# Kernel tuning notes

Hardware: AMD Instinct MI355X
Metric: run time of the kernel (lower is better)

The kernel has to match this reference:

```python
import jax, jax.numpy as jnp
import numpy as np

B, DIN, NU, N, ORDER = 256, 64, 256, 207, 3
KC = (ORDER + 1) * (DIN + NU)  # 1280 concat channels into gate conv
SQRT_D = float(np.sqrt(NU))


def layer_norm(x, w, b, eps=1e-5):
    mu = jnp.mean(x, -1, keepdims=True)
    var = jnp.mean((x - mu) ** 2, -1, keepdims=True)
    return (x - mu) / jnp.sqrt(var + eps) * w + b


def spatial_diffusion(x, adj, order):
    # x: (B, C, N). Order-K diffusion with self term, matching SpatialConvOrderK:
    # x_k[..., w] = sum_v adj[w, v] * x_{k-1}[..., v]
    outs = [x]
    xk = x
    for _ in range(order):
        xk = jnp.einsum('bcv,wv->bcw', xk, adj)
        outs.append(xk)
    return jnp.concatenate(outs, axis=1)  # (B, (order+1)*C, N)


def transformer_layer(s, in_proj_w, in_proj_b, out_proj_w, out_proj_b,
                      ln1_w, ln1_b, ln2_w, ln2_b, ffn_w1, ffn_b1, ffn_w2, ffn_b2):
    # s: (N, B, d). Single-head post-LN TransformerEncoderLayer, eval mode (dropout off).
    qkv = s @ in_proj_w.T + in_proj_b
    q, k, v = jnp.split(qkv, 3, axis=-1)
    attn = jax.nn.softmax(jnp.einsum('nbd,mbd->bnm', q, k) / SQRT_D, axis=-1)
    o = jnp.einsum('bnm,mbd->nbd', attn, v) @ out_proj_w.T + out_proj_b
    s = layer_norm(s + o, ln1_w, ln1_b)
    f = jax.nn.relu(s @ ffn_w1.T + ffn_b1) @ ffn_w2.T + ffn_b2
    return layer_norm(s + f, ln2_w, ln2_b)


def gcgru_forward(x, delta_t, h, adj, mask_last_tp, embed,
                  in_proj_w, in_proj_b, out_proj_w, out_proj_b,
                  ln1_w, ln1_b, ln2_w, ln2_b, ffn_w1, ffn_b1, ffn_w2, ffn_b2,
                  W_u, b_u, W_c, b_c, step):
    if step != 0:
        h_p = jnp.transpose(h, (2, 0, 1))  # (N, B, NU)
        inp = h_p + embed[:, None, :] * jnp.transpose(mask_last_tp, (2, 0, 1))  # (N,B,1) bcast
        eps = jnp.tanh(transformer_layer(inp, in_proj_w, in_proj_b, out_proj_w, out_proj_b,
                                         ln1_w, ln1_b, ln2_w, ln2_b,
                                         ffn_w1, ffn_b1, ffn_w2, ffn_b2))
        eps = jnp.transpose(eps, (1, 2, 0))  # (B, NU, N)
        dt = delta_t[..., None]  # (B, 1, 1)
        h = jnp.sqrt(1.0 - dt) * h - jnp.sqrt(dt) * eps
    xg = jnp.concatenate([x, h], axis=1)  # (B, DIN+NU, N)
    # update_gate and c_gate receive the identical concat -> compute diffusion once
    z = spatial_diffusion(xg, adj, ORDER)  # (B, KC, N)
    u = jax.nn.sigmoid(jnp.einsum('bcn,oc->bon', z, W_u) + b_u[None, :, None])
    c = jnp.tanh(jnp.einsum('bcn,oc->bon', z, W_c) + b_c[None, :, None])
    return u * h + (1.0 - u) * c


def setup_inputs() -> dict:
    key = jax.random.key(0)
    ks = jax.random.split(key, 16)
    d = NU

    def nrm(k, shape, s=0.02):
        return jax.random.normal(k, shape, jnp.float32) * s

    return dict(
        x=jax.random.normal(ks[0], (B, DIN, N), jnp.float32),
        delta_t=jax.random.uniform(ks[1], (B, 1), jnp.float32, 0.01, 0.99),
        h=jax.random.normal(ks[2], (B, NU, N), jnp.float32),
        adj=jax.random.uniform(ks[3], (N, N), jnp.float32) / N,
        mask=jnp.ones((B, 1, N), jnp.float32),
        mask_last_tp=(jax.random.uniform(ks[4], (B, 1, N)) > 0.5).astype(jnp.float32),
        time_encoding=jnp.zeros((B, d), jnp.float32),
        step=1,
        embed=nrm(ks[5], (N, d), 1.0),
        in_proj_w=nrm(ks[6], (3 * d, d)), in_proj_b=jnp.zeros((3 * d,), jnp.float32),
        out_proj_w=nrm(ks[7], (d, d)), out_proj_b=jnp.zeros((d,), jnp.float32),
        ln1_w=jnp.ones((d,), jnp.float32), ln1_b=jnp.zeros((d,), jnp.float32),
        ln2_w=jnp.ones((d,), jnp.float32), ln2_b=jnp.zeros((d,), jnp.float32),
        ffn_w1=nrm(ks[8], (d, d)), ffn_b1=jnp.zeros((d,), jnp.float32),
        ffn_w2=nrm(ks[9], (d, d)), ffn_b2=jnp.zeros((d,), jnp.float32),
        W_u=nrm(ks[10], (NU, KC)), b_u=jnp.zeros((NU,), jnp.float32),
        W_c=nrm(ks[11], (NU, KC)), b_c=jnp.zeros((NU,), jnp.float32),
    )


def reference(x, delta_t, h, adj, mask, mask_last_tp, time_encoding, step,
              embed, in_proj_w, in_proj_b, out_proj_w, out_proj_b,
              ln1_w, ln1_b, ln2_w, ln2_b, ffn_w1, ffn_b1, ffn_w2, ffn_b2,
              W_u, b_u, W_c, b_c):
    # mask / time_encoding are accepted but unused, exactly as in the torch epsilon.forward
    return gcgru_forward(x, delta_t, h, adj, mask_last_tp, embed,
                         in_proj_w, in_proj_b, out_proj_w, out_proj_b,
                         ln1_w, ln1_b, ln2_w, ln2_b, ffn_w1, ffn_b1, ffn_w2, ffn_b2,
                         W_u, b_u, W_c, b_c, step)
```

## Files before the change

### kernel.cpp

```cpp
#include <hip/hip_runtime.h>
#include <hip/hip_bf16.h>

typedef __hip_bfloat16 bf16;
typedef __attribute__((ext_vector_type(8))) short s8v;
typedef __attribute__((ext_vector_type(4))) short s4v;
typedef __attribute__((ext_vector_type(4))) float f4v;

#define MFMA(a, b, c) __builtin_amdgcn_mfma_f32_16x16x32_bf16(a, b, c, 0, 0, 0)

#define B_    256
#define DIN_  64
#define NU_   256
#define NN_   207
#define KC_   1280
#define NB_   (NN_ * B_)
#define NBD_  13565952LL

#define WU_OFF   0LL
#define WC_OFF   327680LL
#define IP_OFF   655360LL
#define OP_OFF   851968LL
#define F1_OFF   917504LL
#define F2_OFF   983040LL
#define ADJ_OFF  1048576LL
#define WEXT_N   (ADJ_OFF + 207LL * 256LL)

__device__ __forceinline__ float bf2f(bf16 v) { return __bfloat162float(v); }
__device__ __forceinline__ bf16  f2bf(float v) { return __float2bfloat16(v); }
__device__ __forceinline__ short f2s(float v) { bf16 t = __float2bfloat16(v); return *(short*)&t; }

__device__ __forceinline__ void gl16(const void* g, void* l) {
    __builtin_amdgcn_global_load_lds(
        (const __attribute__((address_space(1))) void*)g,
        (__attribute__((address_space(3))) void*)l, 16, 0, 0);
}

#define SWZ(rr, cb) ((rr) * 64 + ((((cb) + q) ^ ((rr) & 7)) << 3))

__global__ __launch_bounds__(256) void cvt_w_k(
    const float* __restrict__ Wu, const float* __restrict__ Wc,
    const float* __restrict__ ip, const float* __restrict__ op,
    const float* __restrict__ f1, const float* __restrict__ f2,
    const float* __restrict__ adj, short* __restrict__ dst)
{
    long long t = (long long)blockIdx.x * 256 + threadIdx.x;
    long long nt = (long long)gridDim.x * 256;
    for (long long g = t; g < 262144; g += nt) {
        long long e = g * 4;
        const float* src; long long off;
        if (e < WC_OFF)      { src = Wu; off = e; }
        else if (e < IP_OFF) { src = Wc; off = e - WC_OFF; }
        else if (e < OP_OFF) { src = ip; off = e - IP_OFF; }
        else if (e < F1_OFF) { src = op; off = e - OP_OFF; }
        else if (e < F2_OFF) { src = f1; off = e - F1_OFF; }
        else                 { src = f2; off = e - F2_OFF; }
        float4 fv = *(const float4*)(src + off);
        s4v v = {f2s(fv.x), f2s(fv.y), f2s(fv.z), f2s(fv.w)};
        *(s4v*)(dst + e) = v;
    }
    short* adst = dst + ADJ_OFF;
    for (long long g = t; g < 207LL * 256LL; g += nt) {
        int r = (int)(g >> 8), c = (int)(g & 255);
        adst[g] = (c < NN_) ? f2s(adj[r * NN_ + c]) : (short)0;
    }
}

template<int EPI>
__global__ __launch_bounds__(256, 3) void gemm128(
    const short* __restrict__ A, int lda,
    const short* __restrict__ Wb, int ldb,
    const float* __restrict__ bias, bf16* __restrict__ C, int ldc,
    int K, int act, short* __restrict__ vt,
    const float* __restrict__ bu, const float* __restrict__ bc,
    const bf16* __restrict__ hnT, float* __restrict__ outF)
{
    __shared__ __align__(16) short Tiles[2][128 * 64];
    short* As = Tiles[0];
    short* Bs = Tiles[1];
    float* outS = (float*)&Tiles[0][0];
    const int w_ = blockIdx.y * gridDim.x + blockIdx.x;
    const int nswz = gridDim.x;
    const int xr = w_ & 7, sidx = w_ >> 3;
    const int mt = xr + 8 * (sidx / nswz);
    const int nt = sidx % nswz;
    if (mt >= 414) return;
    const int m0 = mt * 128, n0 = nt * 128;
    const int tid = threadIdx.x;
    const int lane = tid & 63, wid = tid >> 6;
    const int l15 = lane & 15, q = lane >> 4;
    const int wm = (wid >> 1) * 64, wn = (wid & 1) * 64;
    const int seg_r = lane >> 3;
    const int csw8 = ((lane & 7) ^ seg_r) << 3;
    const int nk = K >> 6;

    const short* ap[4];
    const short* bp[4];
#pragma unroll
    for (int i = 0; i < 4; i++) {
        int gm = m0 + (wid * 4 + i) * 8 + seg_r;
        ap[i] = A + (long long)gm * lda + csw8;
        int gn = n0 + (wid * 4 + i) * 8 + seg_r;
        int pr = EPI ? ((gn & 1) * 256 + (gn >> 1)) : gn;
        bp[i] = Wb + (long long)pr * ldb + csw8;
    }

    f4v acc[4][4] = {};

    for (int t = 0; t < nk; ++t) {
        const int k0 = t << 6;
#pragma unroll
        for (int i = 0; i < 4; i++) {
            gl16(ap[i] + k0, &As[(wid * 4 + i) * 512]);
            gl16(bp[i] + k0, &Bs[(wid * 4 + i) * 512]);
        }
        __syncthreads();
#pragma unroll
        for (int ks = 0; ks < 64; ks += 32) {
            const int cb = ks >> 3;
            s8v af[4], bfv[4];
#pragma unroll
            for (int i = 0; i < 4; i++) {
                int rr = wm + i * 16 + l15;
                af[i] = *(const s8v*)&As[SWZ(rr, cb)];
            }
#pragma unroll
            for (int j = 0; j < 4; j++) {
                int rr = wn + j * 16 + l15;
                bfv[j] = *(const s8v*)&Bs[SWZ(rr, cb)];
            }
#pragma unroll
            for (int i = 0; i < 4; i++)
#pragma unroll
                for (int j = 0; j < 4; j++)
                    acc[i][j] = MFMA(af[i], bfv[j], acc[i][j]);
        }
        __syncthreads();
    }

    if (EPI == 0) {
#pragma unroll
        for (int i = 0; i < 4; i++) {
            int mbase = m0 + wm + i * 16 + q * 4;
#pragma unroll
            for (int j = 0; j < 4; j++) {
                int n = n0 + wn + j * 16 + l15;
                float bv = bias ? bias[n] : 0.f;
#pragma unroll
                for (int r = 0; r < 4; r++) {
                    int m = mbase + r;
                    float v = acc[i][j][r] + bv;
                    if (act == 3) v = fmaxf(v, 0.f);
                    if (vt && n >= 512) {
                        int d = n - 512;
                        int bb = m / NN_;
                        int node = m - bb * NN_;
                        vt[((long long)bb * 256 + d) * 208 + node] = f2s(v);
                    } else {
                        C[(long long)m * ldc + n] = f2bf(v);
                    }
                }
            }
        }
    } else {
        const int odd = l15 & 1;
#pragma unroll
        for (int i = 0; i < 4; i++) {
            int mlbase = wm + i * 16 + q * 4;
#pragma unroll
            for (int j = 0; j < 4; j++) {
                int n = n0 + wn + j * 16 + l15;
                int och = n >> 1;
                int ochl = (wn + j * 16 + l15) >> 1;
                float bv = odd ? bc[och] : bu[och];
#pragma unroll
                for (int r = 0; r < 4; r++) {
                    int ml = mlbase + r;
                    float pre = acc[i][j][r] + bv;
                    float myv;
                    if (odd) {
                        float e = __expf(2.f * pre);
                        myv = (e - 1.f) / (e + 1.f);
                    } else {
                        myv = 1.f / (1.f + __expf(-pre));
                    }
                    float oth = __shfl_xor(myv, 1);
                    if (!odd) {
                        int m = m0 + ml;
                        float hv = bf2f(hnT[(long long)m * 256 + och]);
                        float res = myv * hv + (1.f - myv) * oth;
                        outS[ochl * 128 + (ml ^ ((ochl & 7) << 2))] = res;
                    }
                }
            }
        }
        __syncthreads();
        for (int orow = tid >> 6; orow < 64; orow += 4) {
            int och = (n0 >> 1) + orow;
            const int sx = (orow & 7) << 2;
#pragma unroll
            for (int half = 0; half < 2; half++) {
                int ml = lane + half * 64;
                float v = outS[orow * 128 + (ml ^ sx)];
                int m = m0 + ml;
                int bb = m / NN_;
                int node = m - bb * NN_;
                outF[((long long)bb * NU_ + och) * NN_ + node] = v;
            }
        }
    }
}

__global__ __launch_bounds__(256) void gemm_nk0(
    const short* __restrict__ A, int lda,
    const float* __restrict__ Wf, int ldb,
    const float* __restrict__ bias, bf16* __restrict__ C, int ldc,
    int M, int N, int K, int act, short* __restrict__ vt)
{
    __shared__ __align__(16) short As[2][128 * 64];
    __shared__ __align__(16) short Bs[2][128 * 64];
    const int tid = threadIdx.x;
    const int lane = tid & 63, wid = tid >> 6;
    const int l15 = lane & 15, q = lane >> 4;
    const int wm = (wid >> 1) * 64, wn = (wid & 1) * 64;
    const int m0 = blockIdx.y * 128, n0 = blockIdx.x * 128;

    f4v acc[4][4] = {};
    const int nk = K >> 6;

    auto stage = [&](int k0, int pb) {
#pragma unroll
        for (int i = 0; i < 4; i++) {
            int idx = tid + (i << 8);
            int r = idx >> 3, c = idx & 7;
            int gm = m0 + r, gk = k0 + (c << 3);
            s8v v = {0, 0, 0, 0, 0, 0, 0, 0};
            if (gm < M) v = *(const s8v*)(A + (long long)gm * lda + gk);
            *(s8v*)&As[pb][r * 64 + ((c ^ (r & 7)) << 3)] = v;
        }
#pragma unroll
        for (int i = 0; i < 8; i++) {
            int idx = tid + (i << 8);
            int r = idx >> 4, c4 = idx & 15;
            int gn = n0 + r, gk = k0 + (c4 << 2);
            s4v v = {0, 0, 0, 0};
            if (gn < N) {
                float4 fx = *(const float4*)(Wf + (long long)gn * ldb + gk);
                v[0] = f2s(fx.x); v[1] = f2s(fx.y); v[2] = f2s(fx.z); v[3] = f2s(fx.w);
            }
            *(s4v*)&Bs[pb][r * 64 + (((c4 >> 1) ^ (r & 7)) << 3) + ((c4 & 1) << 2)] = v;
        }
    };

    stage(0, 0);
    __syncthreads();
    int pp = 0;
    for (int t = 0; t < nk; ++t) {
        if (t + 1 < nk) stage((t + 1) << 6, pp ^ 1);
#pragma unroll
        for (int ks = 0; ks < 64; ks += 32) {
            const int cb = ks >> 3;
            s8v af[4], bfv[4];
#pragma unroll
            for (int i = 0; i < 4; i++) {
                int rr = wm + i * 16 + l15;
                af[i] = *(const s8v*)&As[pp][SWZ(rr, cb)];
            }
#pragma unroll
            for (int j = 0; j < 4; j++) {
                int rr = wn + j * 16 + l15;
                bfv[j] = *(const s8v*)&Bs[pp][SWZ(rr, cb)];
            }
#pragma unroll
            for (int i = 0; i < 4; i++)
#pragma unroll
                for (int j = 0; j < 4; j++)
                    acc[i][j] = MFMA(af[i], bfv[j], acc[i][j]);
        }
        __syncthreads();
        pp ^= 1;
    }

#pragma unroll
    for (int i = 0; i < 4; i++) {
        int mbase = m0 + wm + i * 16 + q * 4;
#pragma unroll
        for (int j = 0; j < 4; j++) {
            int n = n0 + wn + j * 16 + l15;
            if (n >= N) continue;
            float bv = bias ? bias[n] : 0.f;
#pragma unroll
            for (int r = 0; r < 4; r++) {
                int m = mbase + r;
                if (m >= M) continue;
                float v = acc[i][j][r] + bv;
                if (act == 3) v = fmaxf(v, 0.f);
                if (vt && n >= 512) {
                    int d = n - 512;
                    int bb = m / NN_;
                    int node = m - bb * NN_;
                    vt[((long long)bb * 256 + d) * 208 + node] = f2s(v);
                } else {
                    C[(long long)m * ldc + n] = f2bf(v);
                }
            }
        }
    }
}

__global__ __launch_bounds__(256) void attn_k(
    const short* __restrict__ qk, const short* __restrict__ vt,
    bf16* __restrict__ ao)
{
    __shared__ __align__(16) short Plds[64 * 232];
    __shared__ float sums[64];
    const int tid = threadIdx.x;
    const int lane = tid & 63, w = tid >> 6;
    const int l15 = lane & 15, quad = lane >> 4;
    const int w_ = blockIdx.y * gridDim.x + blockIdx.x;
    const int xr = w_ & 7, sidx = w_ >> 3;
    const int b = xr + 8 * (sidx >> 2);
    const int q0 = (sidx & 3) * 64;
    const long long rowcap = (long long)NB_ - 1;

    long long qrow = (long long)b * NN_ + q0 + w * 16 + l15;
    if (qrow > rowcap) qrow = rowcap;
    const short* qp = qk + qrow * 512;
    s8v bq[8];
#pragma unroll
    for (int ks = 0; ks < 8; ks++)
        bq[ks] = *(const s8v*)(qp + ks * 32 + quad * 8);

    const short* jp[13];
#pragma unroll
    for (int jf = 0; jf < 13; jf++) {
        long long jrow = (long long)b * NN_ + jf * 16 + l15;
        if (jrow > rowcap) jrow = rowcap;
        jp[jf] = qk + jrow * 512 + 256;
    }

    f4v sacc[13] = {};
#pragma unroll
    for (int ks = 0; ks < 8; ks++) {
        const int off = ks * 32 + quad * 8;
#pragma unroll
        for (int jf = 0; jf < 13; jf++) {
            s8v a = *(const s8v*)(jp[jf] + off);
            sacc[jf] = MFMA(a, bq[ks], sacc[jf]);
        }
    }

    float mx = -3.0e38f;
    float pv[13][4];
#pragma unroll
    for (int jf = 0; jf < 13; jf++)
#pragma unroll
        for (int r = 0; r < 4; r++) {
            int j = jf * 16 + quad * 4 + r;
            float v = (j < NN_) ? sacc[jf][r] * 0.0625f : -3.0e38f;
            pv[jf][r] = v;
            mx = fmaxf(mx, v);
        }
    mx = fmaxf(mx, __shfl_xor(mx, 16));
    mx = fmaxf(mx, __shfl_xor(mx, 32));
    float sum = 0.f;
#pragma unroll
    for (int jf = 0; jf < 13; jf++)
#pragma unroll
        for (int r = 0; r < 4; r++) {
            float p = __expf(pv[jf][r] - mx);
            pv[jf][r] = p;
            sum += p;
        }
    sum += __shfl_xor(sum, 16);
    sum += __shfl_xor(sum, 32);

    const int qloc = w * 16 + l15;
#pragma unroll
    for (int jf = 0; jf < 13; jf++)
#pragma unroll
        for (int r = 0; r < 4; r++)
            Plds[qloc * 232 + jf * 16 + quad * 4 + r] = f2s(pv[jf][r]);
    if (quad == 0) sums[qloc] = 1.f / sum;
#pragma unroll
    for (int i = 0; i < 4; i++) {
        int u = tid + i * 256;
        Plds[(u >> 4) * 232 + 208 + (u & 15)] = 0;
    }
    __syncthreads();

    const short* vbase = vt + (long long)b * 256 * 208;
    f4v oacc[16] = {};
#pragma unroll
    for (int ks = 0; ks < 7; ks++) {
        s8v pa = *(const s8v*)&Plds[(w * 16 + l15) * 232 + ks * 32 + quad * 8];
#pragma unroll
        for (int df = 0; df < 16; df++) {
            s8v vb = *(const s8v*)(vbase + (df * 16 + l15) * 208 + ks * 32 + quad * 8);
            oacc[df] = MFMA(pa, vb, oacc[df]);
        }
    }

#pragma unroll
    for (int df = 0; df < 16; df++) {
        int d = df * 16 + l15;
#pragma unroll
        for (int r = 0; r < 4; r++) {
            int ql = w * 16 + quad * 4 + r;
            int qg = q0 + ql;
            if (qg < NN_)
                ao[((long long)b * NN_ + qg) * 256 + d] = f2bf(oacc[df][r] * sums[ql]);
        }
    }
}

template<int WB>
__global__ __launch_bounds__(256) void diff_k(
    const float* __restrict__ adj, const short* __restrict__ adjb,
    const short* __restrict__ zT_in,
    short* __restrict__ zT_out, int col_in, int col_out)
{
    __shared__ __align__(16) short As[2][128 * 64];
    __shared__ __align__(16) short Bs[2][128 * 64];
    const int tid = threadIdx.x;
    const int lane = tid & 63, wid = tid >> 6;
    const int l15 = lane & 15, q = lane >> 4;
    const int wm = (wid >> 1) * 64, wn = (wid & 1) * 64;
    const int m0 = blockIdx.y * 128, n0 = blockIdx.x * 128;
    const long long zb = (long long)blockIdx.z * NN_ * KC_;
    const int seg_r = lane >> 3, chunk = lane & 7;
    const int csw8 = (chunk ^ seg_r) << 3;
    const int bv_ = tid & 63, bcg = tid >> 6;

    f4v acc[4][4] = {};

    auto stageA = [&](int k0, int pb) {
        if (WB) {
#pragma unroll
            for (int i = 0; i < 4; i++) {
                int seg = wid * 4 + i;
                int gm = m0 + seg * 8 + seg_r;
                if (gm > NN_ - 1) gm = NN_ - 1;
                gl16(adjb + gm * 256 + k0 + csw8, &As[pb][seg * 512]);
            }
        } else {
#pragma unroll
            for (int i = 0; i < 32; i++) {
                int idx = tid + (i << 8);
                int r = idx >> 6, c = idx & 63;
                int gm = m0 + r, gk = k0 + c;
                short vv = (gm < NN_ && gk < NN_) ? f2s(adj[gm * NN_ + gk]) : (short)0;
                As[pb][r * 64 + (((c >> 3) ^ (r & 7)) << 3) + (c & 7)] = vv;
            }
        }
    };
    auto loadB = [&](int k0, s8v* breg) {
#pragma unroll
        for (int i = 0; i < 4; i++) {
            int gv = k0 + bv_, gc = n0 + (bcg + i * 4) * 8;
            s8v val = {0, 0, 0, 0, 0, 0, 0, 0};
            if (gv < NN_ && gc < 320)
                val = *(const s8v*)&zT_in[zb + (long long)gv * KC_ + col_in + gc];
            breg[i] = val;
        }
    };
    auto writeB = [&](s8v* breg, int pb) {
#pragma unroll
        for (int i = 0; i < 4; i++) {
            int cg = bcg + i * 4;
#pragma unroll
            for (int e = 0; e < 8; e++) {
                int row = cg * 8 + e;
                Bs[pb][row * 64 + (((bv_ >> 3) ^ (row & 7)) << 3) + (bv_ & 7)] = breg[i][e];
            }
        }
    };

    s8v breg[4];
    loadB(0, breg);
    stageA(0, 0);
    writeB(breg, 0);
    __syncthreads();
    int pp = 0;
    for (int t = 0; t < 4; ++t) {
        if (t < 3) { loadB((t + 1) << 6, breg); stageA((t + 1) << 6, pp ^ 1); }
#pragma unroll
        for (int ks = 0; ks < 64; ks += 32) {
            const int cb = ks >> 3;
            s8v af[4], bfv[4];
#pragma unroll
            for (int i = 0; i < 4; i++) {
                int rr = wm + i * 16 + l15;
                af[i] = *(const s8v*)&As[pp][SWZ(rr, cb)];
            }
#pragma unroll
            for (int j = 0; j < 4; j++) {
                int rr = wn + j * 16 + l15;
                bfv[j] = *(const s8v*)&Bs[pp][SWZ(rr, cb)];
            }
#pragma unroll
            for (int i = 0; i < 4; i++)
#pragma unroll
                for (int j = 0; j < 4; j++)
                    acc[i][j] = MFMA(af[i], bfv[j], acc[i][j]);
        }
        if (t < 3) writeB(breg, pp ^ 1);
        __syncthreads();
        pp ^= 1;
    }

#pragma unroll
    for (int i = 0; i < 4; i++) {
        int mbase = m0 + wm + i * 16 + q * 4;
#pragma unroll
        for (int j = 0; j < 4; j++) {
            int n = n0 + wn + j * 16 + l15;
            if (n >= 320) continue;
#pragma unroll
            for (int r = 0; r < 4; r++) {
                int m = mbase + r;
                if (m >= NN_) continue;
                zT_out[zb + (long long)m * KC_ + col_out + n] = f2s(acc[i][j][r]);
            }
        }
    }
}

__global__ __launch_bounds__(256) void gates_k0(
    const short* __restrict__ zT, const float* __restrict__ Wu,
    const float* __restrict__ Wc, const float* __restrict__ bu,
    const float* __restrict__ bc, const bf16* __restrict__ hnT,
    float* __restrict__ out)
{
    __shared__ __align__(16) short As[2][128 * 64];
    __shared__ __align__(16) short Bu[2][64 * 64];
    __shared__ __align__(16) short Bc[2][64 * 64];
    const int tid = threadIdx.x;
    const int lane = tid & 63, wid = tid >> 6;
    const int l15 = lane & 15, q = lane >> 4;
    const int b = blockIdx.z;
    const int m0 = blockIdx.y * 128;
    const int n0 = blockIdx.x * 64;
    const long long zb = (long long)b * NN_ * KC_;

    f4v aU[2][4] = {}, aC[2][4] = {};

    auto stage = [&](int k0, int pb) {
#pragma unroll
        for (int i = 0; i < 4; i++) {
            int idx = tid + (i << 8);
            int r = idx >> 3, c = idx & 7;
            int gw = m0 + r;
            s8v v = {0, 0, 0, 0, 0, 0, 0, 0};
            if (gw < NN_) v = *(const s8v*)&zT[zb + (long long)gw * KC_ + k0 + (c << 3)];
            *(s8v*)&As[pb][r * 64 + ((c ^ (r & 7)) << 3)] = v;
        }
#pragma unroll
        for (int i = 0; i < 4; i++) {
            int idx = tid + (i << 8);
            int r = idx >> 4, c4 = idx & 15;
            long long widx = (long long)(n0 + r) * KC_ + k0 + (c4 << 2);
            float4 fu = *(const float4*)(Wu + widx);
            float4 fc = *(const float4*)(Wc + widx);
            s4v vu = {f2s(fu.x), f2s(fu.y), f2s(fu.z), f2s(fu.w)};
            s4v vc = {f2s(fc.x), f2s(fc.y), f2s(fc.z), f2s(fc.w)};
            int di = r * 64 + (((c4 >> 1) ^ (r & 7)) << 3) + ((c4 & 1) << 2);
            *(s4v*)&Bu[pb][di] = vu;
            *(s4v*)&Bc[pb][di] = vc;
        }
    };

    stage(0, 0);
    __syncthreads();
    int pp = 0;
    for (int t = 0; t < 20; ++t) {
        if (t < 19) stage((t + 1) << 6, pp ^ 1);
#pragma unroll
        for (int ks = 0; ks < 64; ks += 32) {
            const int cb = ks >> 3;
            s8v af[2], bfu[4], bfc[4];
#pragma unroll
            for (int i = 0; i < 2; i++) {
                int rr = wid * 32 + i * 16 + l15;
                af[i] = *(const s8v*)&As[pp][SWZ(rr, cb)];
            }
#pragma unroll
            for (int j = 0; j < 4; j++) {
                int rr = j * 16 + l15;
                bfu[j] = *(const s8v*)&Bu[pp][SWZ(rr, cb)];
                bfc[j] = *(const s8v*)&Bc[pp][SWZ(rr, cb)];
            }
#pragma unroll
            for (int i = 0; i < 2; i++)
#pragma unroll
                for (int j = 0; j < 4; j++) {
                    aU[i][j] = MFMA(af[i], bfu[j], aU[i][j]);
                    aC[i][j] = MFMA(af[i], bfc[j], aC[i][j]);
                }
        }
        __syncthreads();
        pp ^= 1;
    }

#pragma unroll
    for (int i = 0; i < 2; i++) {
        int wbase = m0 + wid * 32 + i * 16 + q * 4;
#pragma unroll
        for (int j = 0; j < 4; j++) {
            int och = n0 + j * 16 + l15;
            float bvu = bu[och];
            float bvc = bc[och];
#pragma unroll
            for (int r = 0; r < 4; r++) {
                int w = wbase + r;
                if (w >= NN_) continue;
                float u = 1.f / (1.f + __expf(-(aU[i][j][r] + bvu)));
                float cg = tanhf(aC[i][j][r] + bvc);
                float hv = bf2f(hnT[((long long)b * NN_ + w) * 256 + och]);
                out[((long long)b * NU_ + och) * NN_ + w] = u * hv + (1.f - u) * cg;
            }
        }
    }
}

__global__ __launch_bounds__(256) void build_inp_k(
    const float* __restrict__ h, const float* __restrict__ embed,
    const float* __restrict__ mlt, bf16* __restrict__ inp)
{
    __shared__ float t[32][33];
    const int b = blockIdx.z;
    const int n0 = blockIdx.x * 32, c0 = blockIdx.y * 32;
    const int t5 = threadIdx.x & 31, t8 = threadIdx.x >> 5;
#pragma unroll
    for (int r = 0; r < 4; r++) {
        int c = c0 + t8 + r * 8;
        int n = n0 + t5;
        t[t8 + r * 8][t5] = (n < NN_) ? h[((long long)b * 256 + c) * NN_ + n] : 0.f;
    }
    __syncthreads();
#pragma unroll
    for (int r = 0; r < 4; r++) {
        int n = n0 + t8 + r * 8;
        int c = c0 + t5;
        if (n < NN_) {
            float v = t[t5][t8 + r * 8] + embed[n * 256 + c] * mlt[b * NN_ + n];
            inp[((long long)b * NN_ + n) * 256 + c] = f2bf(v);
        }
    }
}

__global__ __launch_bounds__(256) void add_ln_k(
    const bf16* __restrict__ xr, const bf16* __restrict__ yr,
    const float* __restrict__ w, const float* __restrict__ bb,
    bf16* __restrict__ out, int do_tanh)
{
    const int lane = threadIdx.x & 63, wv = threadIdx.x >> 6;
    const long long row = (long long)blockIdx.x * 4 + wv;
    const long long base = row * 256 + lane * 4;
    s4v xv = *(const s4v*)((const short*)xr + base);
    s4v yv = *(const s4v*)((const short*)yr + base);
    float v[4];
    float sum = 0.f;
#pragma unroll
    for (int i = 0; i < 4; i++) {
        short sx = xv[i], sy = yv[i];
        v[i] = bf2f(*(bf16*)&sx) + bf2f(*(bf16*)&sy);
        sum += v[i];
    }
#pragma unroll
    for (int s = 1; s < 64; s <<= 1) sum += __shfl_xor(sum, s);
    float mu = sum * (1.f / 256.f);
    float vs = 0.f;
#pragma unroll
    for (int i = 0; i < 4; i++) { float d = v[i] - mu; vs += d * d; }
#pragma unroll
    for (int s = 1; s < 64; s <<= 1) vs += __shfl_xor(vs, s);
    float inv = rsqrtf(vs * (1.f / 256.f) + 1e-5f);
    s4v ov;
#pragma unroll
    for (int i = 0; i < 4; i++) {
        float r = (v[i] - mu) * inv * w[lane * 4 + i] + bb[lane * 4 + i];
        if (do_tanh) r = tanhf(r);
        ov[i] = f2s(r);
    }
    *(s4v*)((short*)out + base) = ov;
}

__global__ __launch_bounds__(256) void hnew_k(
    const float* __restrict__ h, const bf16* __restrict__ epsb,
    const float* __restrict__ dt, const int* __restrict__ step, bf16* __restrict__ hnT)
{
    __shared__ float t[32][33];
    const int b = blockIdx.z;
    const int n0 = blockIdx.x * 32, c0 = blockIdx.y * 32;
    const int t5 = threadIdx.x & 31, t8 = threadIdx.x >> 5;
#pragma unroll
    for (int r = 0; r < 4; r++) {
        int c = c0 + t8 + r * 8;
        int n = n0 + t5;
        t[t8 + r * 8][t5] = (n < NN_) ? h[((long long)b * 256 + c) * NN_ + n] : 0.f;
    }
    __syncthreads();
    const int st = *step;
    const float d = dt[b];
    const float sa = sqrtf(fmaxf(1.f - d, 0.f)), sb = sqrtf(d);
#pragma unroll
    for (int r = 0; r < 4; r++) {
        int n = n0 + t8 + r * 8;
        int c = c0 + t5;
        if (n < NN_) {
            float hv = t[t5][t8 + r * 8];
            float val = hv;
            if (st != 0) {
                float ev = bf2f(epsb[((long long)b * NN_ + n) * 256 + c]);
                val = sa * hv - sb * ev;
            }
            hnT[((long long)b * NN_ + n) * 256 + c] = f2bf(val);
        }
    }
}

__global__ __launch_bounds__(256) void zx_k(
    const float* __restrict__ x, short* __restrict__ zT)
{
    __shared__ float t[32][33];
    const int b = blockIdx.z;
    const int n0 = blockIdx.x * 32, c0 = blockIdx.y * 32;
    const int t5 = threadIdx.x & 31, t8 = threadIdx.x >> 5;
#pragma unroll
    for (int r = 0; r < 4; r++) {
        int c = c0 + t8 + r * 8;
        int n = n0 + t5;
        t[t8 + r * 8][t5] = (n < NN_) ? x[((long long)b * DIN_ + c) * NN_ + n] : 0.f;
    }
    __syncthreads();
#pragma unroll
    for (int r = 0; r < 4; r++) {
        int n = n0 + t8 + r * 8;
        int c = c0 + t5;
        if (n < NN_)
            zT[((long long)b * NN_ + n) * KC_ + c] = f2s(t[t5][t8 + r * 8]);
    }
}

__global__ __launch_bounds__(256) void zcopy_k(
    const short* __restrict__ hnT, short* __restrict__ zT)
{
    long long u = (long long)blockIdx.x * 256 + threadIdx.x;
    long long row = u >> 5;
    int cu = (int)(u & 31);
    s8v v = *(const s8v*)(hnT + row * 256 + cu * 8);
    *(s8v*)(zT + row * KC_ + 64 + cu * 8) = v;
}

extern "C" void kernel_launch(void* const* d_in, const int* in_sizes, int n_in,
                              void* d_out, int out_size, void* d_ws, size_t ws_size,
                              hipStream_t stream) {
    const float* x          = (const float*)d_in[0];
    const float* delta_t    = (const float*)d_in[1];
    const float* h          = (const float*)d_in[2];
    const float* adj        = (const float*)d_in[3];
    const float* mlt        = (const float*)d_in[5];
    const int*  step        = (const int*)d_in[7];
    const float* embed      = (const float*)d_in[8];
    const float* in_proj_w  = (const float*)d_in[9];
    const float* in_proj_b  = (const float*)d_in[10];
    const float* out_proj_w = (const float*)d_in[11];
    const float* out_proj_b = (const float*)d_in[12];
    const float* ln1_w      = (const float*)d_in[13];
    const float* ln1_b      = (const float*)d_in[14];
    const float* ln2_w      = (const float*)d_in[15];
    const float* ln2_b      = (const float*)d_in[16];
    const float* ffn_w1     = (const float*)d_in[17];
    const float* ffn_b1     = (const float*)d_in[18];
    const float* ffn_w2     = (const float*)d_in[19];
    const float* ffn_b2     = (const float*)d_in[20];
    const float* W_u        = (const float*)d_in[21];
    const float* b_u        = (const float*)d_in[22];
    const float* W_c        = (const float*)d_in[23];
    const float* b_c        = (const float*)d_in[24];
    float* out = (float*)d_out;
    bf16* ws   = (bf16*)d_ws;

    bf16* inp = ws;
    short* qk = (short*)(ws + 1 * NBD_);
    short* vt = (short*)(ws + 3 * NBD_);
    bf16* ao  = ws + 4 * NBD_ + 65536;
    bf16* o   = ws + 1 * NBD_;
    bf16* s   = ws + 2 * NBD_;
    bf16* f   = ws + 1 * NBD_;
    bf16* f2  = ws + 3 * NBD_;
    bf16* eps = ws + 2 * NBD_;
    bf16* hnT = ws;
    short* zT = (short*)(ws + 1 * NBD_);
    short* wext = (short*)(ws + 6 * NBD_);

    const size_t need = (size_t)(6 * NBD_ + WEXT_N) * 2;
    const bool fast = ws_size >= need;

    short* wuc  = wext + WU_OFF;
    short* ipb  = wext + IP_OFF;
    short* opb  = wext + OP_OFF;
    short* f1b  = wext + F1_OFF;
    short* f2b  = wext + F2_OFF;
    short* adjb = wext + ADJ_OFF;

    if (fast)
        cvt_w_k<<<dim3(1024), dim3(256), 0, stream>>>(
            W_u, W_c, in_proj_w, out_proj_w, ffn_w1, ffn_w2, adj, wext);

    build_inp_k<<<dim3(7, 8, 256), dim3(256), 0, stream>>>(h, embed, mlt, inp);

    if (fast)
        gemm128<0><<<dim3(6, 416), dim3(256), 0, stream>>>(
            (const short*)inp, 256, ipb, 256, in_proj_b,
            (bf16*)qk, 512, 256, 0, vt, nullptr, nullptr, nullptr, nullptr);
    else
        gemm_nk0<<<dim3(6, 414), dim3(256), 0, stream>>>(
            (const short*)inp, 256, in_proj_w, 256, in_proj_b,
            (bf16*)qk, 512, NB_, 768, 256, 0, vt);

    attn_k<<<dim3(4, 256), dim3(256), 0, stream>>>(qk, vt, ao);

    if (fast)
        gemm128<0><<<dim3(2, 416), dim3(256), 0, stream>>>(
            (const short*)ao, 256, opb, 256, out_proj_b,
            o, 256, 256, 0, nullptr, nullptr, nullptr, nullptr, nullptr);
    else
        gemm_nk0<<<dim3(2, 414), dim3(256), 0, stream>>>(
            (const short*)ao, 256, out_proj_w, 256, out_proj_b, o, 256, NB_, 256, 256, 0, nullptr);

    add_ln_k<<<dim3(NB_ / 4), dim3(256), 0, stream>>>(inp, o, ln1_w, ln1_b, s, 0);

    if (fast)
        gemm128<0><<<dim3(2, 416), dim3(256), 0, stream>>>(
            (const short*)s, 256, f1b, 256, ffn_b1,
            f, 256, 256, 3, nullptr, nullptr, nullptr, nullptr, nullptr);
    else
        gemm_nk0<<<dim3(2, 414), dim3(256), 0, stream>>>(
            (const short*)s, 256, ffn_w1, 256, ffn_b1, f, 256, NB_, 256, 256, 3, nullptr);

    if (fast)
        gemm128<0><<<dim3(2, 416), dim3(256), 0, stream>>>(
            (const short*)f, 256, f2b, 256, ffn_b2,
            f2, 256, 256, 0, nullptr, nullptr, nullptr, nullptr, nullptr);
    else
        gemm_nk0<<<dim3(2, 414), dim3(256), 0, stream>>>(
            (const short*)f, 256, ffn_w2, 256, ffn_b2, f2, 256, NB_, 256, 256, 0, nullptr);

    add_ln_k<<<dim3(NB_ / 4), dim3(256), 0, stream>>>(s, f2, ln2_w, ln2_b, eps, 1);

    hnew_k<<<dim3(7, 8, 256), dim3(256), 0, stream>>>(h, eps, delta_t, step, hnT);

    zx_k<<<dim3(7, 2, 256), dim3(256), 0, stream>>>(x, zT);
    zcopy_k<<<dim3(6624), dim3(256), 0, stream>>>((const short*)hnT, zT);

    if (fast) {
        diff_k<1><<<dim3(3, 2, 256), dim3(256), 0, stream>>>(adj, adjb, zT, zT, 0, 320);
        diff_k<1><<<dim3(3, 2, 256), dim3(256), 0, stream>>>(adj, adjb, zT, zT, 320, 640);
        diff_k<1><<<dim3(3, 2, 256), dim3(256), 0, stream>>>(adj, adjb, zT, zT, 640, 960);
    } else {
        diff_k<0><<<dim3(3, 2, 256), dim3(256), 0, stream>>>(adj, nullptr, zT, zT, 0, 320);
        diff_k<0><<<dim3(3, 2, 256), dim3(256), 0, stream>>>(adj, nullptr, zT, zT, 320, 640);
        diff_k<0><<<dim3(3, 2, 256), dim3(256), 0, stream>>>(adj, nullptr, zT, zT, 640, 960);
    }

    if (fast)
        gemm128<1><<<dim3(4, 416), dim3(256), 0, stream>>>(
            zT, KC_, wuc, KC_, nullptr,
            nullptr, 0, KC_, 0, nullptr, b_u, b_c, hnT, out);
    else
        gates_k0<<<dim3(4, 2, 256), dim3(256), 0, stream>>>(
            zT, W_u, W_c, b_u, b_c, hnT, out);

    (void)in_sizes; (void)n_in; (void)out_size; (void)ws_size;
}
```

Before: 710.1 us.

## Stage K and V tiles through swizzled LDS in attention kernel

The attention kernel now loads K rows and V-transpose slices cooperatively into a shared LDS buffer using 16-byte direct global-to-LDS loads with XOR swizzling. All four waves then read their MFMA operands from LDS instead of each wave fetching the same K/V data from global memory. This reduces redundant global and L2 traffic but adds a barrier per chunk and extra LDS use, with launch bounds set to target three blocks per SM.

```diff
diff --git a/kernel.cpp b/kernel.cpp
--- a/kernel.cpp
+++ b/kernel.cpp
@@ -307,10 +307,11 @@
     }
 }
 
-__global__ __launch_bounds__(256) void attn_k(
+__global__ __launch_bounds__(256, 3) void attn_k(
     const short* __restrict__ qk, const short* __restrict__ vt,
     bf16* __restrict__ ao)
 {
+    __shared__ __align__(16) short KV[8192];
     __shared__ __align__(16) short Plds[64 * 232];
     __shared__ float sums[64];
     const int tid = threadIdx.x;
@@ -321,8 +322,9 @@
     const int b = xr + 8 * (sidx >> 2);
     const int q0 = (sidx & 3) * 64;
     const long long rowcap = (long long)NB_ - 1;
-
-    long long qrow = (long long)b * NN_ + q0 + w * 16 + l15;
+    const long long bbase = (long long)b * NN_;
+
+    long long qrow = bbase + q0 + w * 16 + l15;
     if (qrow > rowcap) qrow = rowcap;
     const short* qp = qk + qrow * 512;
     s8v bq[8];
@@ -330,23 +332,33 @@
     for (int ks = 0; ks < 8; ks++)
         bq[ks] = *(const s8v*)(qp + ks * 32 + quad * 8);
 
-    const short* jp[13];
-#pragma unroll
-    for (int jf = 0; jf < 13; jf++) {
-        long long jrow = (long long)b * NN_ + jf * 16 + l15;
-        if (jrow > rowcap) jrow = rowcap;
-        jp[jf] = qk + jrow * 512 + 256;
-    }
-
     f4v sacc[13] = {};
-#pragma unroll
-    for (int ks = 0; ks < 8; ks++) {
-        const int off = ks * 32 + quad * 8;
-#pragma unroll
-        for (int jf = 0; jf < 13; jf++) {
-            s8v a = *(const s8v*)(jp[jf] + off);
-            sacc[jf] = MFMA(a, bq[ks], sacc[jf]);
-        }
+    const int sr2 = lane >> 5;
+    const int c32 = lane & 31;
+#pragma unroll
+    for (int jc = 0; jc < 7; ++jc) {
+#pragma unroll
+        for (int i = 0; i < 4; i++) {
+            int lrow = w * 8 + i * 2 + sr2;
+            int jrow = jc * 32 + lrow;
+            if (jrow > NN_ - 1) jrow = NN_ - 1;
+            gl16(qk + (bbase + jrow) * 512 + 256 + ((c32 ^ (lrow & 7)) << 3),
+                 &KV[(w * 8 + i * 2) * 256]);
+        }
+        __syncthreads();
+#pragma unroll
+        for (int jf2 = 0; jf2 < 2; jf2++) {
+            const int jf = jc * 2 + jf2;
+            if (jf < 13) {
+                const int lrow = jf2 * 16 + l15;
+#pragma unroll
+                for (int ks = 0; ks < 8; ks++) {
+                    s8v a = *(const s8v*)&KV[lrow * 256 + (((ks * 4 + quad) ^ (lrow & 7)) << 3)];
+                    sacc[jf] = MFMA(a, bq[ks], sacc[jf]);
+                }
+            }
+        }
+        __syncthreads();
     }
 
     float mx = -3.0e38f;
@@ -390,14 +402,24 @@
 
     const short* vbase = vt + (long long)b * 256 * 208;
     f4v oacc[16] = {};
-#pragma unroll
+    const int vr = lane >> 2;
+    const int vc = lane & 3;
     for (int ks = 0; ks < 7; ks++) {
+#pragma unroll
+        for (int i = 0; i < 4; i++) {
+            int d = w * 64 + i * 16 + vr;
+            gl16(vbase + (long long)d * 208 + ks * 32 + ((vc ^ ((d >> 1) & 3)) << 3),
+                 &KV[(w * 64 + i * 16) * 32]);
+        }
+        __syncthreads();
         s8v pa = *(const s8v*)&Plds[(w * 16 + l15) * 232 + ks * 32 + quad * 8];
 #pragma unroll
         for (int df = 0; df < 16; df++) {
-            s8v vb = *(const s8v*)(vbase + (df * 16 + l15) * 208 + ks * 32 + quad * 8);
+            const int dl = df * 16 + l15;
+            s8v vb = *(const s8v*)&KV[dl * 32 + ((quad ^ ((dl >> 1) & 3)) << 3)];
             oacc[df] = MFMA(pa, vb, oacc[df]);
         }
+        __syncthreads();
     }
 
 #pragma unroll
```

Measured after the change: 674.5 us. -5.0%, faster.
